# Kernel optimization log

Measured on AMD Instinct MI355X. Metric: run time of the kernel, lower is better.

## Reference

```python
import jax, jax.numpy as jnp
import numpy as np
import math

SR = 96000.0
FRAME = 2048
NB = 16
GAIN_RANGE = (-24.0, 24.0)
Q_RANGE = (0.5, 16.0)
BROADBAND = (-60.0, 0.0)
HPF_R = (20.0, 500.0)
LPF_R = (5000.0, 20000.0)
SHELF_R = (50.0, 16000.0)
PEAK_R = (100.0, 15000.0)


def _dfreq(n, rng):
    lo, hi = math.log(rng[0]), math.log(rng[1])
    return jnp.exp(lo + n * (hi - lo))


def _dgain(n, rng=GAIN_RANGE):
    return rng[0] + n * (rng[1] - rng[0])


def _dq(n):
    lo, hi = math.log(Q_RANGE[0]), math.log(Q_RANGE[1])
    return jnp.exp(lo + n * (hi - lo))


def _coeffs(ftype, fc, gain_db, Q):
    # returns stacked [g, k, a1, a2, a3, m0, m1, m2], each same shape as fc
    g = jnp.clip(jnp.tan(math.pi * fc / SR), 1e-6, 100.0)
    Q = jnp.clip(Q, 0.1, 100.0)
    one = jnp.ones_like(g)
    zero = jnp.zeros_like(g)
    if ftype in ('highpass', 'lowpass'):
        k = 1.0 / Q
        a1 = 1.0 / (1.0 + g * (g + k)); a2 = g * a1; a3 = g * a2
        if ftype == 'highpass':
            m0, m1, m2 = one, -k, -one
        else:
            m0, m1, m2 = zero, zero, one
    elif ftype == 'peak':
        A = jnp.power(10.0, gain_db / 40.0)
        k = jnp.where(gain_db >= 0, 1.0 / (Q * A), A / Q)
        a1 = 1.0 / (1.0 + g * (g + k)); a2 = g * a1; a3 = g * a2
        m0, m1, m2 = one, k * (A * A - 1.0), zero
    elif ftype == 'lowshelf':
        A = jnp.power(10.0, gain_db / 40.0); sA = jnp.sqrt(A); k = 1.0 / Q
        gs = jnp.where(gain_db >= 0, g / sA, g * sA)
        a1 = 1.0 / (1.0 + gs * (gs + k)); a2 = gs * a1; a3 = gs * a2
        m0, m1, m2 = one, k * (A - 1.0), A * A - 1.0
    else:  # highshelf
        A = jnp.power(10.0, gain_db / 40.0); sA = jnp.sqrt(A); k = 1.0 / Q
        gs = jnp.where(gain_db >= 0, g * sA, g / sA)
        a1 = 1.0 / (1.0 + gs * (gs + k)); a2 = gs * a1; a3 = gs * a2
        m0, m1, m2 = A * A, k * (1.0 - A) * A, 1.0 - A * A
    return jnp.stack([g, k, a1, a2, a3, m0, m1, m2], 0)


def _all_coeffs(params, n_frames_audio):
    # params: (B, 50, n_frames_params) -> coeffs (nF, NB, 8, B), in/out gains (nF, B)
    B = params.shape[0]
    nFp = params.shape[2]
    pidx = jnp.minimum(jnp.arange(n_frames_audio), nFp - 1)
    fp = jnp.take(params, pidx, axis=2)                 # (B, 50, nF)
    bq = fp[:, :NB * 3, :].reshape(B, NB, 3, n_frames_audio)
    in_g = jnp.power(10.0, _dgain(fp[:, -2, :], BROADBAND) / 20.0)   # (B, nF)
    out_g = jnp.power(10.0, _dgain(fp[:, -1, :], BROADBAND) / 20.0)  # (B, nF)
    cs = []
    for i in range(NB):
        fn, gn, qn = bq[:, i, 0], bq[:, i, 1], bq[:, i, 2]  # (B, nF)
        Q = _dq(qn)
        if i == 0:
            c = _coeffs('highpass', _dfreq(fn, HPF_R), None, Q)
        elif i == 15:
            c = _coeffs('lowpass', _dfreq(fn, LPF_R), None, Q)
        elif i == 1:
            c = _coeffs('lowshelf', _dfreq(fn, SHELF_R), _dgain(gn), Q)
        elif i == 14:
            c = _coeffs('highshelf', _dfreq(fn, SHELF_R), _dgain(gn), Q)
        else:
            c = _coeffs('peak', _dfreq(fn, PEAK_R), _dgain(gn), Q)
        cs.append(c)  # (8, B, nF)
    coeffs = jnp.transpose(jnp.stack(cs, 0), (3, 0, 1, 2))  # (nF, NB, 8, B)
    return coeffs, in_g.T, out_g.T


def _forward(audio, params):
    B, S = audio.shape
    nF = S // FRAME  # S chosen as exact multiple of FRAME
    coeffs, in_g, out_g = _all_coeffs(params, nF)
    frames = jnp.transpose(audio.reshape(B, nF, FRAME), (1, 2, 0))  # (nF, FRAME, B)

    def frame_step(states, xs):
        fr, c, ig, og = xs  # fr (FRAME,B), c (NB,8,B), ig (B,), og (B,)
        x = fr * ig[None, :]
        new_states = []
        for i in range(NB):
            a1, a2, a3 = c[i, 2], c[i, 3], c[i, 4]
            m0, m1, m2 = c[i, 5], c[i, 6], c[i, 7]

            def samp(st, xn, a1=a1, a2=a2, a3=a3, m0=m0, m1=m1, m2=m2):
                ic1, ic2 = st
                v3 = xn - ic2
                v1 = a1 * ic1 + a2 * v3
                v2 = ic2 + a2 * v1 + a3 * v3
                out = m0 * xn + m1 * v1 + m2 * v2
                return (2.0 * v1 - ic1, 2.0 * v2 - ic2), out

            (ic1, ic2), x = jax.lax.scan(samp, (states[i, 0], states[i, 1]), x)
            new_states.append(jnp.stack([ic1, ic2], 0))
        return jnp.stack(new_states, 0), x * og[None, :]

    init = jnp.zeros((NB, 2, B), audio.dtype)
    _, out = jax.lax.scan(frame_step, init, (frames, coeffs, in_g, out_g))
    return jnp.transpose(out, (2, 0, 1)).reshape(B, S)  # (B, S)


_forward_jit = jax.jit(_forward)


def setup_inputs() -> dict:
    key = jax.random.key(0)
    k1, k2 = jax.random.split(key)
    B, S, nFp = 32, 49152, 24  # 24 frames of 2048 samples
    audio = jax.random.normal(k1, (B, S), dtype=jnp.float32) * 0.1
    params = jax.random.uniform(k2, (B, 50, nFp), dtype=jnp.float32)
    return {'audio': audio, 'params': params}


def reference(audio, params):
    return _forward_jit(audio, params)
```

## Files before the change

### kernel.cpp

```cpp
#include <hip/hip_runtime.h>
#include <math.h>

#define NBATCH 32
#define S      49152
#define NF     24
#define NB     16
#define NBLK   4
#define CHUNK  16
#define NCH    768
#define NWAVE  12

__device__ __forceinline__ float clampf(float x, float lo, float hi) {
    return fminf(fmaxf(x, lo), hi);
}

#define FOREACH_S(OP) \
    OP(s00) OP(s01) OP(s02) OP(s03) OP(s04) OP(s05) OP(s06) OP(s07) \
    OP(s08) OP(s09) OP(s10) OP(s11) OP(s12) OP(s13) OP(s14) OP(s15)

#define DECL_S(x) float x;

#define STEPA(x) { \
    const float n1_ = fmaf(t00, ic1, fmaf(t01, ic2, b0 * (x))); \
    const float n2_ = fmaf(t10, ic1, fmaf(t11, ic2, b1 * (x))); \
    ic1 = n1_; ic2 = n2_; }

#define STEPC(x) { \
    const float y_  = fmaf(c0, ic1, fmaf(c1, ic2, c2 * (x))); \
    const float n1_ = fmaf(t00, ic1, fmaf(t01, ic2, b0 * (x))); \
    const float n2_ = fmaf(t10, ic1, fmaf(t11, ic2, b1 * (x))); \
    (x) = y_; ic1 = n1_; ic2 = n2_; }

__global__ __launch_bounds__(NCH, 3)
void biquad_chain_kernel(const float* __restrict__ audio,
                         const float* __restrict__ params,
                         float* __restrict__ out,
                         unsigned int* __restrict__ ws)
{
    __shared__ __align__(16) float sc[NB][NF][16];
    __shared__ float4 sMw[NB][6];
    __shared__ float4 sPm[NB][NWAVE];
    __shared__ float4 sWm[NB][3];
    __shared__ float4 sT2048[NB][NF];
    __shared__ float  sgain[2][NF];
    __shared__ float2 sagg[2][NWAVE];
    __shared__ float2 sS0;
    __shared__ unsigned int sflag[NB];

    const int t       = threadIdx.x;
    const int xcd     = blockIdx.x & 7;
    const int slot_   = blockIdx.x >> 3;
    const int bt      = xcd * 4 + (slot_ & 3);
    const int quarter = slot_ >> 2;
    const int lane    = t & 63;
    const int wave    = t >> 6;
    const int frame   = quarter * 6 + (wave >> 1);

    if (t < NB * NF) {
        const int f  = t / NF;
        const int fr = t % NF;
        const float* P = params + (size_t)bt * 50 * NF;
        const float fn = P[(3 * f + 0) * NF + fr];
        const float gn = P[(3 * f + 1) * NF + fr];
        const float qn = P[(3 * f + 2) * NF + fr];

        float Q = __expf(-0.69314718f + qn * 3.4657359f);
        Q = clampf(Q, 0.1f, 100.0f);

        float lo, hi;
        int type;
        if      (f == 0)  { lo = 20.0f;   hi = 500.0f;   type = 0; }
        else if (f == 15) { lo = 5000.0f; hi = 20000.0f; type = 1; }
        else if (f == 1)  { lo = 50.0f;   hi = 16000.0f; type = 3; }
        else if (f == 14) { lo = 50.0f;   hi = 16000.0f; type = 4; }
        else              { lo = 100.0f;  hi = 15000.0f; type = 2; }

        const float fc = __expf(__logf(lo) + fn * (__logf(hi) - __logf(lo)));
        float g_ = __tanf((float)M_PI * fc / 96000.0f);
        g_ = clampf(g_, 1e-6f, 100.0f);
        const float gdb = -24.0f + 48.0f * gn;

        float a1, a2, a3, m0, m1, m2;
        if (type == 0 || type == 1) {
            const float k = 1.0f / Q;
            a1 = 1.0f / (1.0f + g_ * (g_ + k)); a2 = g_ * a1; a3 = g_ * a2;
            if (type == 0) { m0 = 1.0f; m1 = -k;   m2 = -1.0f; }
            else           { m0 = 0.0f; m1 = 0.0f; m2 = 1.0f;  }
        } else if (type == 2) {
            const float A = __expf(gdb * (2.30258509f / 40.0f));
            const float k = (gdb >= 0.0f) ? 1.0f / (Q * A) : A / Q;
            a1 = 1.0f / (1.0f + g_ * (g_ + k)); a2 = g_ * a1; a3 = g_ * a2;
            m0 = 1.0f; m1 = k * (A * A - 1.0f); m2 = 0.0f;
        } else {
            const float A  = __expf(gdb * (2.30258509f / 40.0f));
            const float sA = sqrtf(A);
            const float k  = 1.0f / Q;
            float gs;
            if (type == 3) gs = (gdb >= 0.0f) ? g_ / sA : g_ * sA;
            else           gs = (gdb >= 0.0f) ? g_ * sA : g_ / sA;
            a1 = 1.0f / (1.0f + gs * (gs + k)); a2 = gs * a1; a3 = gs * a2;
            if (type == 3) { m0 = 1.0f;  m1 = k * (A - 1.0f);      m2 = A * A - 1.0f; }
            else           { m0 = A * A; m1 = k * (1.0f - A) * A;  m2 = 1.0f - A * A; }
        }

        const float q2  = a2 * a2 + a3;
        const float t00 = 2.0f * a1 - 1.0f;
        const float t01 = -2.0f * a2;
        const float t10 = 2.0f * a1 * a2;
        const float t11 = 1.0f - 2.0f * q2;
        const float b0  = 2.0f * a2;
        const float b1  = 2.0f * q2;
        const float c0  = a1 * (m1 + m2 * a2);
        const float c1  = m2 * (1.0f - q2) - m1 * a2;
        const float c2  = m0 + m1 * a2 + m2 * q2;

        float u00 = t00, u01 = t01, u10 = t10, u11 = t11;
        #pragma unroll
        for (int i = 0; i < 4; i++) {
            const float n00 = u00 * u00 + u01 * u10;
            const float n01 = u00 * u01 + u01 * u11;
            const float n10 = u10 * u00 + u11 * u10;
            const float n11 = u10 * u01 + u11 * u11;
            u00 = n00; u01 = n01; u10 = n10; u11 = n11;
        }
        sc[f][fr][0] = t00; sc[f][fr][1] = t01; sc[f][fr][2] = t10; sc[f][fr][3] = t11;
        sc[f][fr][4] = b0;  sc[f][fr][5] = b1;  sc[f][fr][6] = c0;  sc[f][fr][7] = c1;
        sc[f][fr][8] = c2;  sc[f][fr][9] = u00; sc[f][fr][10] = u01; sc[f][fr][11] = u10;
        sc[f][fr][12] = u11;

        #pragma unroll
        for (int i = 0; i < 6; i++) {
            const float n00 = u00 * u00 + u01 * u10;
            const float n01 = u00 * u01 + u01 * u11;
            const float n10 = u10 * u00 + u11 * u10;
            const float n11 = u10 * u01 + u11 * u11;
            u00 = n00; u01 = n01; u10 = n10; u11 = n11;
        }
        const int lfr = fr - quarter * 6;
        if (lfr >= 0 && lfr < 6) {
            sMw[f][lfr] = make_float4(u00, u01, u10, u11);
        }
        {
            const float n00 = u00 * u00 + u01 * u10;
            const float n01 = u00 * u01 + u01 * u11;
            const float n10 = u10 * u00 + u11 * u10;
            const float n11 = u10 * u01 + u11 * u11;
            sT2048[f][fr] = make_float4(n00, n01, n10, n11);
        }
    }
    if (t >= 384 && t < 384 + 2 * NF) {
        const int idx = t - 384;
        const int which = idx / NF;
        const int fr    = idx % NF;
        const float* P = params + (size_t)bt * 50 * NF;
        const float p  = P[(48 + which) * NF + fr];
        const float db = -60.0f + 60.0f * p;
        sgain[which][fr] = __expf(db * (2.30258509f / 20.0f));
    }
    if (t < NB) sflag[t] = 0u;
    __syncthreads();

    if (t < NB) {
        const int f = t;
        float q00 = 1.0f, q01 = 0.0f, q10 = 0.0f, q11 = 1.0f;
        #pragma unroll
        for (int k = 0; k < 6; k++) {
            sPm[f][2 * k] = make_float4(q00, q01, q10, q11);
            const float4 mw = sMw[f][k];
            sPm[f][2 * k + 1] = make_float4(
                mw.x * q00 + mw.y * q10, mw.x * q01 + mw.y * q11,
                mw.z * q00 + mw.w * q10, mw.z * q01 + mw.w * q11);
            const float4 g = sT2048[f][quarter * 6 + k];
            const float n00 = g.x * q00 + g.y * q10;
            const float n01 = g.x * q01 + g.y * q11;
            const float n10 = g.z * q00 + g.w * q10;
            const float n11 = g.z * q01 + g.w * q11;
            q00 = n00; q01 = n01; q10 = n10; q11 = n11;
        }
        if (quarter > 0) {
            float r00 = 1.0f, r01 = 0.0f, r10 = 0.0f, r11 = 1.0f;
            for (int k = quarter - 1; k >= 0; k--) {
                sWm[f][k] = make_float4(r00, r01, r10, r11);
                if (k > 0) {
                    float b00 = 1.0f, b01 = 0.0f, b10 = 0.0f, b11 = 1.0f;
                    #pragma unroll
                    for (int m = 0; m < 6; m++) {
                        const float4 g = sT2048[f][6 * k + m];
                        const float n00 = g.x * b00 + g.y * b10;
                        const float n01 = g.x * b01 + g.y * b11;
                        const float n10 = g.z * b00 + g.w * b10;
                        const float n11 = g.z * b01 + g.w * b11;
                        b00 = n00; b01 = n01; b10 = n10; b11 = n11;
                    }
                    const float n00 = r00 * b00 + r01 * b10;
                    const float n01 = r00 * b01 + r01 * b11;
                    const float n10 = r10 * b00 + r11 * b10;
                    const float n11 = r10 * b01 + r11 * b11;
                    r00 = n00; r01 = n01; r10 = n10; r11 = n11;
                }
            }
        }
    }
    __syncthreads();

    FOREACH_S(DECL_S)
    {
        const float ing = sgain[0][frame];
        const float* base = audio + (size_t)bt * S
                          + (size_t)(quarter * NCH + t) * CHUNK;
        float4 q;
        q = *(const float4*)(base +  0); s00 = q.x*ing; s01 = q.y*ing; s02 = q.z*ing; s03 = q.w*ing;
        q = *(const float4*)(base +  4); s04 = q.x*ing; s05 = q.y*ing; s06 = q.z*ing; s07 = q.w*ing;
        q = *(const float4*)(base +  8); s08 = q.x*ing; s09 = q.y*ing; s10 = q.z*ing; s11 = q.w*ing;
        q = *(const float4*)(base + 12); s12 = q.x*ing; s13 = q.y*ing; s14 = q.z*ing; s15 = q.w*ing;
    }

    #pragma unroll 1
    for (int f = 0; f < NB; f++) {
        const float4 q0 = *(const float4*)&sc[f][frame][0];
        const float4 q1 = *(const float4*)&sc[f][frame][4];
        const float4 q2 = *(const float4*)&sc[f][frame][8];
        const float  M11v = sc[f][frame][12];
        const float t00 = q0.x, t01 = q0.y, t10 = q0.z, t11 = q0.w;
        const float b0  = q1.x, b1  = q1.y, c0  = q1.z, c1  = q1.w;
        const float c2  = q2.x;

        float ic1 = 0.0f, ic2 = 0.0f;
        FOREACH_S(STEPA)

        float Md00 = q2.y, Md01 = q2.z, Md10 = q2.w, Md11 = M11v;
        float Ac0 = ic1, Ac1 = ic2;
        #pragma unroll
        for (int d = 1; d < 64; d <<= 1) {
            const float lc0 = __shfl_up(Ac0, d);
            const float lc1 = __shfl_up(Ac1, d);
            if (lane >= d) {
                Ac0 = fmaf(Md00, lc0, fmaf(Md01, lc1, Ac0));
                Ac1 = fmaf(Md10, lc0, fmaf(Md11, lc1, Ac1));
            }
            const float n00 = Md00 * Md00 + Md01 * Md10;
            const float n01 = Md00 * Md01 + Md01 * Md11;
            const float n10 = Md10 * Md00 + Md11 * Md10;
            const float n11 = Md10 * Md01 + Md11 * Md11;
            Md00 = n00; Md01 = n01; Md10 = n10; Md11 = n11;
        }

        const int buf = f & 1;
        if (lane == 63) sagg[buf][wave] = make_float2(Ac0, Ac1);

        float ce0 = __shfl_up(Ac0, 1);
        float ce1 = __shfl_up(Ac1, 1);
        if (lane == 0) { ce0 = 0.0f; ce1 = 0.0f; }

        __syncthreads();

        const unsigned int tag = (unsigned int)(f + 1);
        unsigned int* stagebase = ws + ((size_t)(bt * NB + f) * NBLK) * 8;

        float Pc0 = 0.0f, Pc1 = 0.0f;
        #pragma unroll
        for (int j = 0; j < NWAVE - 1; j++) {
            if (j < wave) {
                const float2 a = sagg[buf][j];
                const float4 mw = sMw[f][j >> 1];
                const float n0 = fmaf(mw.x, Pc0, fmaf(mw.y, Pc1, a.x));
                const float n1 = fmaf(mw.z, Pc0, fmaf(mw.w, Pc1, a.y));
                Pc0 = n0; Pc1 = n1;
            }
        }

        if (wave == NWAVE - 1 && quarter < NBLK - 1 && lane == 63) {
            const float4 mw = sMw[f][(NWAVE - 1) >> 1];
            const float i0 = fmaf(mw.x, Pc0, fmaf(mw.y, Pc1, Ac0));
            const float i1 = fmaf(mw.z, Pc0, fmaf(mw.w, Pc1, Ac1));
            unsigned int* slot = stagebase + quarter * 8;
            float* dp = (float*)(slot + 1);
            __hip_atomic_store(&dp[0], i0, __ATOMIC_RELAXED, __HIP_MEMORY_SCOPE_AGENT);
            __hip_atomic_store(&dp[1], i1, __ATOMIC_RELAXED, __HIP_MEMORY_SCOPE_AGENT);
            __hip_atomic_store(slot, tag, __ATOMIC_RELEASE, __HIP_MEMORY_SCOPE_AGENT);
        }

        float S0x = 0.0f, S0y = 0.0f;
        if (quarter > 0) {
            if (wave == 0) {
                float ux = 0.0f, uy = 0.0f;
                if (lane < quarter) {
                    unsigned int* slot = stagebase + lane * 8;
                    while (__hip_atomic_load(slot, __ATOMIC_ACQUIRE, __HIP_MEMORY_SCOPE_AGENT) != tag) {
                        __builtin_amdgcn_s_sleep(1);
                    }
                    const float* dp = (const float*)(slot + 1);
                    const float cx = __hip_atomic_load(&dp[0], __ATOMIC_RELAXED, __HIP_MEMORY_SCOPE_AGENT);
                    const float cy = __hip_atomic_load(&dp[1], __ATOMIC_RELAXED, __HIP_MEMORY_SCOPE_AGENT);
                    const float4 w = sWm[f][lane];
                    ux = fmaf(w.x, cx, w.y * cy);
                    uy = fmaf(w.z, cx, w.w * cy);
                }
                S0x = __shfl(ux, 0);
                S0y = __shfl(uy, 0);
                if (quarter > 1) { S0x += __shfl(ux, 1); S0y += __shfl(uy, 1); }
                if (quarter > 2) { S0x += __shfl(ux, 2); S0y += __shfl(uy, 2); }
                if (lane == 0) {
                    sS0 = make_float2(S0x, S0y);
                    __hip_atomic_store(&sflag[f], tag, __ATOMIC_RELEASE,
                                       __HIP_MEMORY_SCOPE_WORKGROUP);
                }
            } else {
                while (__hip_atomic_load(&sflag[f], __ATOMIC_ACQUIRE,
                                         __HIP_MEMORY_SCOPE_WORKGROUP) != tag)
                    __builtin_amdgcn_s_sleep(1);
                const float2 sb = sS0;
                S0x = sb.x; S0y = sb.y;
            }
        }

        const float4 pm = sPm[f][wave];
        const float vx = fmaf(pm.x, S0x, fmaf(pm.y, S0y, Pc0));
        const float vy = fmaf(pm.z, S0x, fmaf(pm.w, S0y, Pc1));

        float w0 = vx, w1 = vy;
        float p00 = q2.y, p01 = q2.z, p10 = q2.w, p11 = M11v;
        #pragma unroll
        for (int b = 0; b < 6; b++) {
            if (lane & (1 << b)) {
                const float nw0 = fmaf(p00, w0, p01 * w1);
                const float nw1 = fmaf(p10, w0, p11 * w1);
                w0 = nw0; w1 = nw1;
            }
            if (b < 5) {
                const float n00 = p00 * p00 + p01 * p10;
                const float n01 = p00 * p01 + p01 * p11;
                const float n10 = p10 * p00 + p11 * p10;
                const float n11 = p10 * p01 + p11 * p11;
                p00 = n00; p01 = n01; p10 = n10; p11 = n11;
            }
        }
        ic1 = w0 + ce0;
        ic2 = w1 + ce1;

        FOREACH_S(STEPC)
    }

    {
        const float og = sgain[1][frame];
        float* base = out + (size_t)bt * S + (size_t)(quarter * NCH + t) * CHUNK;
        float4 q;
        q.x = s00*og; q.y = s01*og; q.z = s02*og; q.w = s03*og; *(float4*)(base +  0) = q;
        q.x = s04*og; q.y = s05*og; q.z = s06*og; q.w = s07*og; *(float4*)(base +  4) = q;
        q.x = s08*og; q.y = s09*og; q.z = s10*og; q.w = s11*og; *(float4*)(base +  8) = q;
        q.x = s12*og; q.y = s13*og; q.z = s14*og; q.w = s15*og; *(float4*)(base + 12) = q;
    }
}

extern "C" void kernel_launch(void* const* d_in, const int* in_sizes, int n_in,
                              void* d_out, int out_size, void* d_ws, size_t ws_size,
                              hipStream_t stream)
{
    const float* audio  = (const float*)d_in[0];
    const float* params = (const float*)d_in[1];
    float* out = (float*)d_out;
    unsigned int* ws = (unsigned int*)d_ws;
    biquad_chain_kernel<<<NBLK * NBATCH, NCH, 0, stream>>>(audio, params, out, ws);
}
```

Baseline: 111.7 us.

## Replace per-stage block barrier with per-wave shared-memory flags for wave aggregates

Removes the workgroup-wide barrier after each biquad stage's wave-level scan. Each wave publishes its aggregate into a per-stage shared slot with a release flag, and later waves spin on acquire flags for only the predecessors they need. Buffers are now indexed per stage instead of double-buffered, so no barrier is needed to reuse them. This lets waves run ahead across stages, but adds spin-wait loops that also consume issue slots.

```diff
diff --git a/kernel.cpp b/kernel.cpp
--- a/kernel.cpp
+++ b/kernel.cpp
@@ -43,8 +43,9 @@
     __shared__ float4 sWm[NB][3];
     __shared__ float4 sT2048[NB][NF];
     __shared__ float  sgain[2][NF];
-    __shared__ float2 sagg[2][NWAVE];
-    __shared__ float2 sS0;
+    __shared__ float2 sagg2[NB][NWAVE];
+    __shared__ unsigned int stag[NB][NWAVE];
+    __shared__ float2 sS0f[NB];
     __shared__ unsigned int sflag[NB];
 
     const int t       = threadIdx.x;
@@ -157,6 +158,7 @@
         const float db = -60.0f + 60.0f * p;
         sgain[which][fr] = __expf(db * (2.30258509f / 20.0f));
     }
+    if (t < NB * NWAVE) stag[t / NWAVE][t % NWAVE] = 0u;
     if (t < NB) sflag[t] = 0u;
     __syncthreads();
 
@@ -245,28 +247,29 @@
             Md00 = n00; Md01 = n01; Md10 = n10; Md11 = n11;
         }
 
-        const int buf = f & 1;
-        if (lane == 63) sagg[buf][wave] = make_float2(Ac0, Ac1);
+        if (lane == 63) {
+            sagg2[f][wave] = make_float2(Ac0, Ac1);
+            __hip_atomic_store(&stag[f][wave], 1u, __ATOMIC_RELEASE,
+                               __HIP_MEMORY_SCOPE_WORKGROUP);
+        }
 
         float ce0 = __shfl_up(Ac0, 1);
         float ce1 = __shfl_up(Ac1, 1);
         if (lane == 0) { ce0 = 0.0f; ce1 = 0.0f; }
 
-        __syncthreads();
-
         const unsigned int tag = (unsigned int)(f + 1);
         unsigned int* stagebase = ws + ((size_t)(bt * NB + f) * NBLK) * 8;
 
         float Pc0 = 0.0f, Pc1 = 0.0f;
-        #pragma unroll
-        for (int j = 0; j < NWAVE - 1; j++) {
-            if (j < wave) {
-                const float2 a = sagg[buf][j];
-                const float4 mw = sMw[f][j >> 1];
-                const float n0 = fmaf(mw.x, Pc0, fmaf(mw.y, Pc1, a.x));
-                const float n1 = fmaf(mw.z, Pc0, fmaf(mw.w, Pc1, a.y));
-                Pc0 = n0; Pc1 = n1;
-            }
+        for (int j = 0; j < wave; j++) {
+            while (__hip_atomic_load(&stag[f][j], __ATOMIC_ACQUIRE,
+                                     __HIP_MEMORY_SCOPE_WORKGROUP) != 1u)
+                __builtin_amdgcn_s_sleep(1);
+            const float2 a = sagg2[f][j];
+            const float4 mw = sMw[f][j >> 1];
+            const float n0 = fmaf(mw.x, Pc0, fmaf(mw.y, Pc1, a.x));
+            const float n1 = fmaf(mw.z, Pc0, fmaf(mw.w, Pc1, a.y));
+            Pc0 = n0; Pc1 = n1;
         }
 
         if (wave == NWAVE - 1 && quarter < NBLK - 1 && lane == 63) {
@@ -301,15 +304,15 @@
                 if (quarter > 1) { S0x += __shfl(ux, 1); S0y += __shfl(uy, 1); }
                 if (quarter > 2) { S0x += __shfl(ux, 2); S0y += __shfl(uy, 2); }
                 if (lane == 0) {
-                    sS0 = make_float2(S0x, S0y);
-                    __hip_atomic_store(&sflag[f], tag, __ATOMIC_RELEASE,
+                    sS0f[f] = make_float2(S0x, S0y);
+                    __hip_atomic_store(&sflag[f], 1u, __ATOMIC_RELEASE,
                                        __HIP_MEMORY_SCOPE_WORKGROUP);
                 }
             } else {
                 while (__hip_atomic_load(&sflag[f], __ATOMIC_ACQUIRE,
-                                         __HIP_MEMORY_SCOPE_WORKGROUP) != tag)
+                                         __HIP_MEMORY_SCOPE_WORKGROUP) != 1u)
                     __builtin_amdgcn_s_sleep(1);
-                const float2 sb = sS0;
+                const float2 sb = sS0f[f];
                 S0x = sb.x; S0y = sb.y;
             }
         }
```

New measurement: 127.9 us. 14.5% more time.

## Compute zero-state outputs in first pass, add initial-state response via precomputed rho

Applied to the files above, without the earlier changes.

The first pass over each chunk now computes zero-initial-state outputs alongside the state. The second serial recurrence pass is replaced by a superposition: each sample gets a correction of rho_k·(ic1,ic2). The rho_k vectors (c·T^k for k<16) are precomputed per filter and frame into shared memory. This removes the second dependent 16-step chain in exchange for extra shared memory and LDS reads per band.

```diff
diff --git a/kernel.cpp b/kernel.cpp
--- a/kernel.cpp
+++ b/kernel.cpp
@@ -20,12 +20,7 @@
 
 #define DECL_S(x) float x;
 
-#define STEPA(x) { \
-    const float n1_ = fmaf(t00, ic1, fmaf(t01, ic2, b0 * (x))); \
-    const float n2_ = fmaf(t10, ic1, fmaf(t11, ic2, b1 * (x))); \
-    ic1 = n1_; ic2 = n2_; }
-
-#define STEPC(x) { \
+#define STEPY(x) { \
     const float y_  = fmaf(c0, ic1, fmaf(c1, ic2, c2 * (x))); \
     const float n1_ = fmaf(t00, ic1, fmaf(t01, ic2, b0 * (x))); \
     const float n2_ = fmaf(t10, ic1, fmaf(t11, ic2, b1 * (x))); \
@@ -42,6 +37,7 @@
     __shared__ float4 sPm[NB][NWAVE];
     __shared__ float4 sWm[NB][3];
     __shared__ float4 sT2048[NB][NF];
+    __shared__ float2 srho[NB][6][16];
     __shared__ float  sgain[2][NF];
     __shared__ float2 sagg[2][NWAVE];
     __shared__ float2 sS0;
@@ -54,7 +50,8 @@
     const int quarter = slot_ >> 2;
     const int lane    = t & 63;
     const int wave    = t >> 6;
-    const int frame   = quarter * 6 + (wave >> 1);
+    const int lf      = wave >> 1;
+    const int frame   = quarter * 6 + lf;
 
     if (t < NB * NF) {
         const int f  = t / NF;
@@ -114,6 +111,20 @@
         const float c1  = m2 * (1.0f - q2) - m1 * a2;
         const float c2  = m0 + m1 * a2 + m2 * q2;
 
+        const int lfr = fr - quarter * 6;
+        const bool loc = (lfr >= 0 && lfr < 6);
+
+        if (loc) {
+            float r0 = c0, r1 = c1;
+            #pragma unroll
+            for (int k = 0; k < 16; k++) {
+                srho[f][lfr][k] = make_float2(r0, r1);
+                const float n0 = r0 * t00 + r1 * t10;
+                const float n1 = r0 * t01 + r1 * t11;
+                r0 = n0; r1 = n1;
+            }
+        }
+
         float u00 = t00, u01 = t01, u10 = t10, u11 = t11;
         #pragma unroll
         for (int i = 0; i < 4; i++) {
@@ -136,8 +147,7 @@
             const float n11 = u10 * u01 + u11 * u11;
             u00 = n00; u01 = n01; u10 = n10; u11 = n11;
         }
-        const int lfr = fr - quarter * 6;
-        if (lfr >= 0 && lfr < 6) {
+        if (loc) {
             sMw[f][lfr] = make_float4(u00, u01, u10, u11);
         }
         {
@@ -226,7 +236,7 @@
         const float c2  = q2.x;
 
         float ic1 = 0.0f, ic2 = 0.0f;
-        FOREACH_S(STEPA)
+        FOREACH_S(STEPY)
 
         float Md00 = q2.y, Md01 = q2.z, Md10 = q2.w, Md11 = M11v;
         float Ac0 = ic1, Ac1 = ic2;
@@ -335,10 +345,26 @@
                 p00 = n00; p01 = n01; p10 = n10; p11 = n11;
             }
         }
-        ic1 = w0 + ce0;
-        ic2 = w1 + ce1;
-
-        FOREACH_S(STEPC)
+        const float icf1 = w0 + ce0;
+        const float icf2 = w1 + ce1;
+
+        const float2* rr = srho[f][lf];
+        { const float2 r = rr[ 0]; s00 = fmaf(r.x, icf1, fmaf(r.y, icf2, s00)); }
+        { const float2 r = rr[ 1]; s01 = fmaf(r.x, icf1, fmaf(r.y, icf2, s01)); }
+        { const float2 r = rr[ 2]; s02 = fmaf(r.x, icf1, fmaf(r.y, icf2, s02)); }
+        { const float2 r = rr[ 3]; s03 = fmaf(r.x, icf1, fmaf(r.y, icf2, s03)); }
+        { const float2 r = rr[ 4]; s04 = fmaf(r.x, icf1, fmaf(r.y, icf2, s04)); }
+        { const float2 r = rr[ 5]; s05 = fmaf(r.x, icf1, fmaf(r.y, icf2, s05)); }
+        { const float2 r = rr[ 6]; s06 = fmaf(r.x, icf1, fmaf(r.y, icf2, s06)); }
+        { const float2 r = rr[ 7]; s07 = fmaf(r.x, icf1, fmaf(r.y, icf2, s07)); }
+        { const float2 r = rr[ 8]; s08 = fmaf(r.x, icf1, fmaf(r.y, icf2, s08)); }
+        { const float2 r = rr[ 9]; s09 = fmaf(r.x, icf1, fmaf(r.y, icf2, s09)); }
+        { const float2 r = rr[10]; s10 = fmaf(r.x, icf1, fmaf(r.y, icf2, s10)); }
+        { const float2 r = rr[11]; s11 = fmaf(r.x, icf1, fmaf(r.y, icf2, s11)); }
+        { const float2 r = rr[12]; s12 = fmaf(r.x, icf1, fmaf(r.y, icf2, s12)); }
+        { const float2 r = rr[13]; s13 = fmaf(r.x, icf1, fmaf(r.y, icf2, s13)); }
+        { const float2 r = rr[14]; s14 = fmaf(r.x, icf1, fmaf(r.y, icf2, s14)); }
+        { const float2 r = rr[15]; s15 = fmaf(r.x, icf1, fmaf(r.y, icf2, s15)); }
     }
 
     {
```

After: 113.0 us. No clear change (+1.1%).
